# Kernel tuning notes

Hardware: AMD Instinct MI355X
Metric: run time of the kernel (lower is better)

## Reference

```python
import jax, jax.numpy as jnp
import numpy as np

B, N, F_ = 4, 2048, 512
H = 8
D = F_ // H


def setup_inputs() -> dict:
    key = jax.random.key(0)
    ks = jax.random.split(key, 9)
    s = 1.0 / np.sqrt(F_)
    return {
        "x": jax.random.normal(ks[0], (B, N, F_), dtype=jnp.float32),
        "Wq": jax.random.normal(ks[1], (F_, F_), dtype=jnp.float32) * s,
        "bq": jax.random.normal(ks[2], (F_,), dtype=jnp.float32) * 0.01,
        "Wk": jax.random.normal(ks[3], (F_, F_), dtype=jnp.float32) * s,
        "bk": jax.random.normal(ks[4], (F_,), dtype=jnp.float32) * 0.01,
        "Wv": jax.random.normal(ks[5], (F_, F_), dtype=jnp.float32) * s,
        "bv": jax.random.normal(ks[6], (F_,), dtype=jnp.float32) * 0.01,
        "Wo": jax.random.normal(ks[7], (F_, F_), dtype=jnp.float32) * s,
        "bo": jax.random.normal(ks[8], (F_,), dtype=jnp.float32) * 0.01,
    }


def reference(x, Wq, bq, Wk, bk, Wv, bv, Wo, bo):
    b, n, f = x.shape
    h, d = H, f // H
    # projections -> [b, h, n, d]
    q = (x @ Wq + bq).reshape(b, n, h, d).transpose(0, 2, 1, 3)
    k = (x @ Wk + bk).reshape(b, n, h, d).transpose(0, 2, 1, 3)
    v = (x @ Wv + bv).reshape(b, n, h, d).transpose(0, 2, 1, 3)
    # NOTE: module scales by sqrt(feats), not sqrt(head_dim)
    sqrt_d = jnp.asarray(f, x.dtype) ** 0.5
    score = jax.nn.softmax(jnp.einsum('bhif,bhjf->bhij', q, k) / sqrt_d, axis=-1)
    attn = jnp.einsum('bhij,bhjf->bihf', score, v).reshape(b, n, f)
    return attn @ Wo + bo
```

## Files before the change

kernel.cpp:

```cpp
#include <hip/hip_runtime.h>


typedef _Float16 f16;
typedef _Float16 f16x2 __attribute__((ext_vector_type(2)));
typedef _Float16 f16x4 __attribute__((ext_vector_type(4)));
typedef _Float16 f16x8 __attribute__((ext_vector_type(8)));
typedef float f32x4 __attribute__((ext_vector_type(4)));

#define MFMA16(a, b, c) __builtin_amdgcn_mfma_f32_16x16x32_f16((a), (b), (c), 0, 0, 0)
#if __has_builtin(__builtin_amdgcn_exp2f)
#define EXP2(x) __builtin_amdgcn_exp2f(x)
#else
#define EXP2(x) exp2f(x)
#endif
#define GLLDS16(gp, lp)                                                    \
  __builtin_amdgcn_global_load_lds(                                        \
      (const __attribute__((address_space(1))) unsigned int*)(gp),         \
      (__attribute__((address_space(3))) unsigned int*)(lp), 16, 0, 0)

#define QSCALE 0.0637587f

__global__ __launch_bounds__(256) void k_cvt_x(const float* __restrict__ x,
                                               f16* __restrict__ xb, int n4) {
  int i = blockIdx.x * 256 + threadIdx.x;
  const int stride = gridDim.x * 256;
  const float4* xp = (const float4*)x;
  f16x4* op = (f16x4*)xb;
  for (; i < n4; i += stride) {
    float4 v = xp[i];
    f16x4 o = {(f16)v.x, (f16)v.y, (f16)v.z, (f16)v.w};
    op[i] = o;
  }
}

__global__ __launch_bounds__(256) void k_cvt_w(const float* __restrict__ Wq,
                                               const float* __restrict__ Wk,
                                               const float* __restrict__ Wv,
                                               const float* __restrict__ Wo,
                                               f16* __restrict__ wt) {
  const int w = blockIdx.y;
  const float* W = (w == 0) ? Wq : (w == 1) ? Wk : (w == 2) ? Wv : Wo;
  const int j0 = (blockIdx.x >> 4) * 32;
  const int k0 = (blockIdx.x & 15) * 32;
  __shared__ float tl[32][33];
  const int tx = threadIdx.x & 31, ty = threadIdx.x >> 5;
#pragma unroll
  for (int i = 0; i < 32; i += 8)
    tl[ty + i][tx] = W[(size_t)(k0 + ty + i) * 512 + j0 + tx];
  __syncthreads();
#pragma unroll
  for (int i = 0; i < 32; i += 8)
    wt[(size_t)w * 262144 + (size_t)(j0 + ty + i) * 512 + (k0 + tx)] =
        (f16)tl[tx][ty + i];
}

template <int BN, int MODE>
__global__ __launch_bounds__(256) void k_gemm(
    const f16* __restrict__ A, const f16* __restrict__ Wb3,
    const float* __restrict__ bias0, const float* __restrict__ bias1,
    const float* __restrict__ bias2, f16* __restrict__ oQ, f16* __restrict__ oK,
    f16* __restrict__ oV, float* __restrict__ oOut) {
  __shared__ __align__(16) f16 a_lds[128 * 64];
  __shared__ __align__(16) f16 b_lds[BN * 64];
  const int t = threadIdx.x;
  const int lane = t & 63, wid = t >> 6;
  const int l15 = lane & 15, l4 = lane >> 4;
  constexpr int MT = (BN == 128) ? 4 : 2;
  const int mbase = (BN == 128) ? (wid >> 1) * 64 : wid * 32;
  const int nbase = (BN == 128) ? (wid & 1) * 64 : 0;
  const int m0 = blockIdx.x * 128;
  const int by = blockIdx.y;
  const int wsel = (MODE == 0) ? (by >> 2) : 0;
  const int n0l = (MODE == 0) ? ((by & 3) * 128) : (by * (BN == 64 ? 64 : 128));
  const f16* Wt = Wb3 + (size_t)wsel * 262144;

  const int srow = t >> 3;
  const int sswz = ((t & 7) ^ (srow & 7)) * 8;
  const f16* Ag = A + (size_t)(m0 + srow) * 512 + sswz;
  const f16* Bg = Wt + (size_t)(n0l + srow) * 512 + sswz;

  f32x4 acc[MT][4];
  const f32x4 z4 = {0.f, 0.f, 0.f, 0.f};
#pragma unroll
  for (int i = 0; i < MT; i++)
#pragma unroll
    for (int j = 0; j < 4; j++) acc[i][j] = z4;

  for (int k0 = 0; k0 < 512; k0 += 64) {
#pragma unroll
    for (int i = 0; i < 4; i++)
      GLLDS16(Ag + (size_t)i * 16384 + k0, &a_lds[i * 2048 + wid * 512]);
#pragma unroll
    for (int i = 0; i < BN / 32; i++)
      GLLDS16(Bg + (size_t)i * 16384 + k0, &b_lds[i * 2048 + wid * 512]);
    __syncthreads();
#pragma unroll
    for (int ks = 0; ks < 2; ks++) {
      const int rs = ((ks * 4 + l4) ^ (l15 & 7)) * 8;
      f16x8 af[MT], bf[4];
#pragma unroll
      for (int mt = 0; mt < MT; mt++)
        af[mt] = *(const f16x8*)&a_lds[(mbase + mt * 16 + l15) * 64 + rs];
#pragma unroll
      for (int nt = 0; nt < 4; nt++)
        bf[nt] = *(const f16x8*)&b_lds[(nbase + nt * 16 + l15) * 64 + rs];
      __builtin_amdgcn_s_setprio(1);
#pragma unroll
      for (int mt = 0; mt < MT; mt++)
#pragma unroll
        for (int nt = 0; nt < 4; nt++)
          acc[mt][nt] = MFMA16(af[mt], bf[nt], acc[mt][nt]);
      __builtin_amdgcn_s_setprio(0);
    }
    __syncthreads();
  }

  if (MODE == 1) {
#pragma unroll
    for (int mt = 0; mt < MT; mt++)
#pragma unroll
      for (int nt = 0; nt < 4; nt++) {
        const int row = m0 + mbase + mt * 16 + l4 * 4;
        const int col = n0l + nbase + nt * 16 + l15;
        const float bv = bias0[col];
#pragma unroll
        for (int r = 0; r < 4; r++)
          oOut[(size_t)(row + r) * 512 + col] = acc[mt][nt][r] + bv;
      }
  } else {
#pragma unroll
    for (int mt = 0; mt < MT; mt++)
#pragma unroll
      for (int nt = 0; nt < 4; nt++) {
        const int colg = by * 128 + nbase + nt * 16 + l15;
        const int w = colg >> 9, jj = colg & 511;
        const int h = jj >> 6, d = jj & 63;
        const float* bp = (w == 0) ? bias0 : (w == 1) ? bias1 : bias2;
        const float bv = bp[jj];
        const float scl = (w == 0) ? QSCALE : 1.0f;
        const int rowg = m0 + mbase + mt * 16 + l4 * 4;
        const int b = rowg >> 11, nn = rowg & 2047;
        if (w == 2) {
          const size_t vb = ((size_t)(b * 8 + h) * 64 + d) * 2048 + nn;
#pragma unroll
          for (int r = 0; r < 4; r++)
            oV[vb + r] = (f16)(acc[mt][nt][r] + bv);
        } else {
          f16* op = (w == 0) ? oQ : oK;
          const size_t base = ((size_t)(b * 8 + h) * 2048 + nn) * 64 + d;
#pragma unroll
          for (int r = 0; r < 4; r++)
            op[base + (size_t)r * 64] = (f16)((acc[mt][nt][r] + bv) * scl);
        }
      }
  }
}

__global__ __launch_bounds__(128, 4) void k_attn(const f16* __restrict__ Q,
                                                 const f16* __restrict__ K,
                                                 const f16* __restrict__ Vt,
                                                 f16* __restrict__ CTX) {
  __shared__ __align__(16) f16 k_lds[2][4096];
  __shared__ __align__(16) f16 v_lds[2][4096];
  const int t = threadIdx.x, wid = t >> 6, lane = t & 63;
  const int l15 = lane & 15, l4 = lane >> 4;
  const int bid = blockIdx.x;
  const int bh = (bid & 7) * 4 + (bid >> 8);
  const int qb = (bid >> 3) & 31;
  const int q0 = qb * 64 + wid * 32;
  const size_t kvb = (size_t)bh * (2048 * 64);

  f16x8 qf[2][2];
#pragma unroll
  for (int g = 0; g < 2; g++)
#pragma unroll
    for (int ks = 0; ks < 2; ks++)
      qf[g][ks] = *(const f16x8*)&Q[kvb + (size_t)(q0 + g * 16 + l15) * 64 +
                                    ks * 32 + l4 * 8];

  f32x4 oa[2][4];
  f32x4 lacc[2];
  const f32x4 z4 = {0.f, 0.f, 0.f, 0.f};
#pragma unroll
  for (int g = 0; g < 2; g++) {
    lacc[g] = z4;
#pragma unroll
    for (int dt = 0; dt < 4; dt++) oa[g][dt] = z4;
  }
  const f16 one = (f16)1.0f;
  const f16x8 ones = {one, one, one, one, one, one, one, one};

  const int kswz = ((lane & 7) ^ (lane >> 3)) * 8;
  const f16* Kgp[4];
  const f16* Vgp[4];
#pragma unroll
  for (int i = 0; i < 4; i++) {
    const int L = i * 16 + wid * 8 + (lane >> 3);
    const int pr = (L & 0x20) | ((L & 0x0C) << 1) | ((L & 0x10) >> 2) | (L & 3);
    Kgp[i] = K + kvb + (size_t)pr * 64 + kswz;
    Vgp[i] = Vt + kvb + (size_t)L * 2048 + kswz;
  }

#pragma unroll
  for (int i = 0; i < 4; i++) {
    GLLDS16(Kgp[i], &k_lds[0][i * 1024 + wid * 512]);
    GLLDS16(Vgp[i], &v_lds[0][i * 1024 + wid * 512]);
  }
  __syncthreads();

  int cur = 0;
  for (int it = 0; it < 32; ++it) {
    if (it < 31) {
      const size_t kb = (size_t)(it + 1) * 4096;
      const size_t vb = (size_t)(it + 1) * 64;
#pragma unroll
      for (int i = 0; i < 4; i++) {
        GLLDS16(Kgp[i] + kb, &k_lds[cur ^ 1][i * 1024 + wid * 512]);
        GLLDS16(Vgp[i] + vb, &v_lds[cur ^ 1][i * 1024 + wid * 512]);
      }
    }

    f32x4 st[2][4];
#pragma unroll
    for (int g = 0; g < 2; g++)
#pragma unroll
      for (int w = 0; w < 4; w++) st[g][w] = z4;
    const f16* kl = k_lds[cur];
#pragma unroll
    for (int ks = 0; ks < 2; ks++) {
      const int rs = ((ks * 4 + l4) ^ (l15 & 7)) * 8;
      f16x8 kf[4];
#pragma unroll
      for (int w = 0; w < 4; w++)
        kf[w] = *(const f16x8*)&kl[(w * 16 + l15) * 64 + rs];
      __builtin_amdgcn_s_setprio(1);
#pragma unroll
      for (int w = 0; w < 4; w++) {
        st[0][w] = MFMA16(kf[w], qf[0][ks], st[0][w]);
        st[1][w] = MFMA16(kf[w], qf[1][ks], st[1][w]);
      }
      __builtin_amdgcn_s_setprio(0);
    }

    f16x8 pa[2][2];
#pragma unroll
    for (int g = 0; g < 2; g++)
#pragma unroll
      for (int ks = 0; ks < 2; ks++) {
        f16x2 a0 = __builtin_bit_cast(
            f16x2, __builtin_amdgcn_cvt_pkrtz(EXP2(st[g][2 * ks][0]),
                                              EXP2(st[g][2 * ks][1])));
        f16x2 a1 = __builtin_bit_cast(
            f16x2, __builtin_amdgcn_cvt_pkrtz(EXP2(st[g][2 * ks][2]),
                                              EXP2(st[g][2 * ks][3])));
        f16x2 a2 = __builtin_bit_cast(
            f16x2, __builtin_amdgcn_cvt_pkrtz(EXP2(st[g][2 * ks + 1][0]),
                                              EXP2(st[g][2 * ks + 1][1])));
        f16x2 a3 = __builtin_bit_cast(
            f16x2, __builtin_amdgcn_cvt_pkrtz(EXP2(st[g][2 * ks + 1][2]),
                                              EXP2(st[g][2 * ks + 1][3])));
        f16x8 p;
        p[0] = a0[0]; p[1] = a0[1]; p[2] = a1[0]; p[3] = a1[1];
        p[4] = a2[0]; p[5] = a2[1]; p[6] = a3[0]; p[7] = a3[1];
        pa[g][ks] = p;
      }

    const f16* vl = v_lds[cur];
#pragma unroll
    for (int ks = 0; ks < 2; ks++) {
      __builtin_amdgcn_s_setprio(1);
      lacc[0] = MFMA16(pa[0][ks], ones, lacc[0]);
      lacc[1] = MFMA16(pa[1][ks], ones, lacc[1]);
#pragma unroll
      for (int dt = 0; dt < 4; dt++) {
        const f16x8 vf = *(const f16x8*)&vl[(dt * 16 + l15) * 64 +
                                            ((ks * 4 + l4) ^ (l15 & 7)) * 8];
        oa[0][dt] = MFMA16(pa[0][ks], vf, oa[0][dt]);
        oa[1][dt] = MFMA16(pa[1][ks], vf, oa[1][dt]);
      }
      __builtin_amdgcn_s_setprio(0);
    }
    __syncthreads();
    cur ^= 1;
  }

  const int b = bh >> 3, h = bh & 7;
#pragma unroll
  for (int g = 0; g < 2; g++)
#pragma unroll
    for (int r = 0; r < 4; r++) {
      const float inv = 1.0f / lacc[g][r];
      const int qrow = q0 + g * 16 + l4 * 4 + r;
#pragma unroll
      for (int dt = 0; dt < 4; dt++)
        CTX[(size_t)(b * 2048 + qrow) * 512 + h * 64 + dt * 16 + l15] =
            (f16)(oa[g][dt][r] * inv);
    }
}

extern "C" void kernel_launch(void* const* d_in, const int* in_sizes, int n_in,
                              void* d_out, int out_size, void* d_ws,
                              size_t ws_size, hipStream_t stream) {
  const float* x = (const float*)d_in[0];
  const float* Wq = (const float*)d_in[1];
  const float* bq = (const float*)d_in[2];
  const float* Wk = (const float*)d_in[3];
  const float* bk = (const float*)d_in[4];
  const float* Wv = (const float*)d_in[5];
  const float* bv = (const float*)d_in[6];
  const float* Wo = (const float*)d_in[7];
  const float* bo = (const float*)d_in[8];
  float* out = (float*)d_out;
  char* ws = (char*)d_ws;

  f16* xb = (f16*)(ws);
  f16* wt = (f16*)(ws + (size_t)(8u << 20));
  f16* Qb = (f16*)(ws + (size_t)(10u << 20));
  f16* Kb = (f16*)(ws + (size_t)(18u << 20));
  f16* Vt = (f16*)(ws + (size_t)(26u << 20));
  f16* CX = (f16*)(ws + (size_t)(34u << 20));

  k_cvt_x<<<dim3(2048), dim3(256), 0, stream>>>(x, xb, 1048576);
  k_cvt_w<<<dim3(256, 4), dim3(256), 0, stream>>>(Wq, Wk, Wv, Wo, wt);
  k_gemm<128, 0><<<dim3(64, 12), dim3(256), 0, stream>>>(
      xb, wt, bq, bk, bv, Qb, Kb, Vt, nullptr);
  k_attn<<<dim3(1024), dim3(128), 0, stream>>>(Qb, Kb, Vt, CX);
  k_gemm<64, 1><<<dim3(64, 8), dim3(256), 0, stream>>>(
      CX, wt + (size_t)3 * 262144, bo, nullptr, nullptr, nullptr, nullptr,
      nullptr, out);
}
```

Measured before the change: 96.95 us.

## Use 4-wave attention blocks with triple-buffered K/V and vmcnt-based waits

The attention kernel now runs 256-thread blocks that each cover 128 query rows, so every K/V tile loaded into LDS serves twice as many queries and the grid halves. K/V staging moves from double to triple buffering with a two-tile prefetch distance. The end-of-iteration __syncthreads is replaced by a partial s_waitcnt vmcnt plus a raw barrier, so the next tile's loads can stay in flight. The cost is more LDS per block (48KB) and fewer resident blocks, and correctness depends on the hand-counted vmcnt value.

```diff
diff --git a/kernel.cpp b/kernel.cpp
--- a/kernel.cpp
+++ b/kernel.cpp
@@ -156,18 +156,18 @@
   }
 }
 
-__global__ __launch_bounds__(128, 4) void k_attn(const f16* __restrict__ Q,
+__global__ __launch_bounds__(256, 2) void k_attn(const f16* __restrict__ Q,
                                                  const f16* __restrict__ K,
                                                  const f16* __restrict__ Vt,
                                                  f16* __restrict__ CTX) {
-  __shared__ __align__(16) f16 k_lds[2][4096];
-  __shared__ __align__(16) f16 v_lds[2][4096];
+  __shared__ __align__(16) f16 k_lds[3][4096];
+  __shared__ __align__(16) f16 v_lds[3][4096];
   const int t = threadIdx.x, wid = t >> 6, lane = t & 63;
   const int l15 = lane & 15, l4 = lane >> 4;
   const int bid = blockIdx.x;
-  const int bh = (bid & 7) * 4 + (bid >> 8);
-  const int qb = (bid >> 3) & 31;
-  const int q0 = qb * 64 + wid * 32;
+  const int bh = (bid & 7) * 4 + (bid >> 7);
+  const int qb = (bid >> 3) & 15;
+  const int q0 = qb * 128 + wid * 32;
   const size_t kvb = (size_t)bh * (2048 * 64);
 
   f16x8 qf[2][2];
@@ -190,34 +190,30 @@
   const f16 one = (f16)1.0f;
   const f16x8 ones = {one, one, one, one, one, one, one, one};
 
+  const int krow = wid * 8 + (lane >> 3);
   const int kswz = ((lane & 7) ^ (lane >> 3)) * 8;
-  const f16* Kgp[4];
-  const f16* Vgp[4];
-#pragma unroll
-  for (int i = 0; i < 4; i++) {
-    const int L = i * 16 + wid * 8 + (lane >> 3);
-    const int pr = (L & 0x20) | ((L & 0x0C) << 1) | ((L & 0x10) >> 2) | (L & 3);
-    Kgp[i] = K + kvb + (size_t)pr * 64 + kswz;
-    Vgp[i] = Vt + kvb + (size_t)L * 2048 + kswz;
-  }
-
-#pragma unroll
-  for (int i = 0; i < 4; i++) {
-    GLLDS16(Kgp[i], &k_lds[0][i * 1024 + wid * 512]);
-    GLLDS16(Vgp[i], &v_lds[0][i * 1024 + wid * 512]);
+  const int kperm = ((krow & 0x0C) << 1) | ((krow & 0x10) >> 2) | (krow & 3);
+  const f16* Kg = K + kvb + (size_t)kperm * 64 + kswz;
+  const f16* Vg = Vt + kvb + (size_t)krow * 2048 + kswz;
+
+#pragma unroll
+  for (int p = 0; p < 2; p++) {
+    GLLDS16(Kg + p * 4096, &k_lds[p][wid * 512]);
+    GLLDS16(Kg + p * 4096 + 2048, &k_lds[p][wid * 512 + 2048]);
+    GLLDS16(Vg + p * 64, &v_lds[p][wid * 512]);
+    GLLDS16(Vg + p * 64 + 32 * 2048, &v_lds[p][wid * 512 + 2048]);
   }
   __syncthreads();
 
-  int cur = 0;
+  int cur = 0, stg = 2;
   for (int it = 0; it < 32; ++it) {
-    if (it < 31) {
-      const size_t kb = (size_t)(it + 1) * 4096;
-      const size_t vb = (size_t)(it + 1) * 64;
-#pragma unroll
-      for (int i = 0; i < 4; i++) {
-        GLLDS16(Kgp[i] + kb, &k_lds[cur ^ 1][i * 1024 + wid * 512]);
-        GLLDS16(Vgp[i] + vb, &v_lds[cur ^ 1][i * 1024 + wid * 512]);
-      }
+    if (it < 30) {
+      const size_t kb = (size_t)(it + 2) * 4096;
+      const size_t vb = (size_t)(it + 2) * 64;
+      GLLDS16(Kg + kb, &k_lds[stg][wid * 512]);
+      GLLDS16(Kg + kb + 2048, &k_lds[stg][wid * 512 + 2048]);
+      GLLDS16(Vg + vb, &v_lds[stg][wid * 512]);
+      GLLDS16(Vg + vb + 32 * 2048, &v_lds[stg][wid * 512 + 2048]);
     }
 
     f32x4 st[2][4];
@@ -225,7 +221,7 @@
     for (int g = 0; g < 2; g++)
 #pragma unroll
       for (int w = 0; w < 4; w++) st[g][w] = z4;
-    const f16* kl = k_lds[cur];
+    const f16* kl = &k_lds[cur][0];
 #pragma unroll
     for (int ks = 0; ks < 2; ks++) {
       const int rs = ((ks * 4 + l4) ^ (l15 & 7)) * 8;
@@ -265,7 +261,7 @@
         pa[g][ks] = p;
       }
 
-    const f16* vl = v_lds[cur];
+    const f16* vl = &v_lds[cur][0];
 #pragma unroll
     for (int ks = 0; ks < 2; ks++) {
       __builtin_amdgcn_s_setprio(1);
@@ -280,8 +276,17 @@
       }
       __builtin_amdgcn_s_setprio(0);
     }
-    __syncthreads();
-    cur ^= 1;
+
+    if (it < 31) {
+      if (it < 30)
+        asm volatile("s_waitcnt vmcnt(4)" ::: "memory");
+      else
+        asm volatile("s_waitcnt vmcnt(0)" ::: "memory");
+      __builtin_amdgcn_s_barrier();
+      __builtin_amdgcn_sched_barrier(0);
+    }
+    cur = (cur == 2) ? 0 : cur + 1;
+    stg = (stg == 2) ? 0 : stg + 1;
   }
 
   const int b = bh >> 3, h = bh & 7;
@@ -324,7 +329,7 @@
   k_cvt_w<<<dim3(256, 4), dim3(256), 0, stream>>>(Wq, Wk, Wv, Wo, wt);
   k_gemm<128, 0><<<dim3(64, 12), dim3(256), 0, stream>>>(
       xb, wt, bq, bk, bv, Qb, Kb, Vt, nullptr);
-  k_attn<<<dim3(1024), dim3(128), 0, stream>>>(Qb, Kb, Vt, CX);
+  k_attn<<<dim3(512), dim3(256), 0, stream>>>(Qb, Kb, Vt, CX);
   k_gemm<64, 1><<<dim3(64, 8), dim3(256), 0, stream>>>(
       CX, wt + (size_t)3 * 262144, bo, nullptr, nullptr, nullptr, nullptr,
       nullptr, out);
```

Measured after the change: 84.66 us. 1.15x faster.

## Split attention KV range into two halves and add a combine kernel

Applied to the files above, without the earlier changes.

Each attention block now uses 4 waves covering 128 query rows and processes only half of the key/value sequence. Unnormalized partial outputs and row sums go to scratch, with the partials stored in the output buffer. A new combine kernel adds the two halves and normalizes before the output projection. The split gives twice as many waves per query tile and halves loop length per block, at the cost of an extra launch, partial-result memory traffic and f16 rounding of unnormalized partials.

```diff
diff --git a/kernel.cpp b/kernel.cpp
--- a/kernel.cpp
+++ b/kernel.cpp
@@ -156,19 +156,22 @@
   }
 }
 
-__global__ __launch_bounds__(128, 4) void k_attn(const f16* __restrict__ Q,
+__global__ __launch_bounds__(256, 4) void k_attn(const f16* __restrict__ Q,
                                                  const f16* __restrict__ K,
                                                  const f16* __restrict__ Vt,
-                                                 f16* __restrict__ CTX) {
+                                                 f16* __restrict__ Op,
+                                                 float* __restrict__ lp) {
   __shared__ __align__(16) f16 k_lds[2][4096];
   __shared__ __align__(16) f16 v_lds[2][4096];
   const int t = threadIdx.x, wid = t >> 6, lane = t & 63;
   const int l15 = lane & 15, l4 = lane >> 4;
   const int bid = blockIdx.x;
-  const int bh = (bid & 7) * 4 + (bid >> 8);
-  const int qb = (bid >> 3) & 31;
-  const int q0 = qb * 64 + wid * 32;
+  const int bh = (bid & 7) * 4 + ((bid >> 7) & 3);
+  const int qb = (bid >> 3) & 15;
+  const int s = bid >> 9;
+  const int q0 = qb * 128 + wid * 32;
   const size_t kvb = (size_t)bh * (2048 * 64);
+  const int kv0 = s * 1024;
 
   f16x8 qf[2][2];
 #pragma unroll
@@ -190,34 +193,27 @@
   const f16 one = (f16)1.0f;
   const f16x8 ones = {one, one, one, one, one, one, one, one};
 
+  const int krow = wid * 8 + (lane >> 3);
   const int kswz = ((lane & 7) ^ (lane >> 3)) * 8;
-  const f16* Kgp[4];
-  const f16* Vgp[4];
-#pragma unroll
-  for (int i = 0; i < 4; i++) {
-    const int L = i * 16 + wid * 8 + (lane >> 3);
-    const int pr = (L & 0x20) | ((L & 0x0C) << 1) | ((L & 0x10) >> 2) | (L & 3);
-    Kgp[i] = K + kvb + (size_t)pr * 64 + kswz;
-    Vgp[i] = Vt + kvb + (size_t)L * 2048 + kswz;
-  }
-
-#pragma unroll
-  for (int i = 0; i < 4; i++) {
-    GLLDS16(Kgp[i], &k_lds[0][i * 1024 + wid * 512]);
-    GLLDS16(Vgp[i], &v_lds[0][i * 1024 + wid * 512]);
-  }
+  const int kperm = ((krow & 0x0C) << 1) | ((krow & 0x10) >> 2) | (krow & 3);
+  const f16* Kg = K + kvb + (size_t)(kv0 + kperm) * 64 + kswz;
+  const f16* Vg = Vt + kvb + (size_t)krow * 2048 + kv0 + kswz;
+
+  GLLDS16(Kg, &k_lds[0][wid * 512]);
+  GLLDS16(Kg + 2048, &k_lds[0][wid * 512 + 2048]);
+  GLLDS16(Vg, &v_lds[0][wid * 512]);
+  GLLDS16(Vg + 32 * 2048, &v_lds[0][wid * 512 + 2048]);
   __syncthreads();
 
   int cur = 0;
-  for (int it = 0; it < 32; ++it) {
-    if (it < 31) {
+  for (int it = 0; it < 16; ++it) {
+    if (it < 15) {
       const size_t kb = (size_t)(it + 1) * 4096;
       const size_t vb = (size_t)(it + 1) * 64;
-#pragma unroll
-      for (int i = 0; i < 4; i++) {
-        GLLDS16(Kgp[i] + kb, &k_lds[cur ^ 1][i * 1024 + wid * 512]);
-        GLLDS16(Vgp[i] + vb, &v_lds[cur ^ 1][i * 1024 + wid * 512]);
-      }
+      GLLDS16(Kg + kb, &k_lds[cur ^ 1][wid * 512]);
+      GLLDS16(Kg + kb + 2048, &k_lds[cur ^ 1][wid * 512 + 2048]);
+      GLLDS16(Vg + vb, &v_lds[cur ^ 1][wid * 512]);
+      GLLDS16(Vg + vb + 32 * 2048, &v_lds[cur ^ 1][wid * 512 + 2048]);
     }
 
     f32x4 st[2][4];
@@ -225,7 +221,7 @@
     for (int g = 0; g < 2; g++)
 #pragma unroll
       for (int w = 0; w < 4; w++) st[g][w] = z4;
-    const f16* kl = k_lds[cur];
+    const f16* kl = &k_lds[cur][0];
 #pragma unroll
     for (int ks = 0; ks < 2; ks++) {
       const int rs = ((ks * 4 + l4) ^ (l15 & 7)) * 8;
@@ -265,7 +261,7 @@
         pa[g][ks] = p;
       }
 
-    const f16* vl = v_lds[cur];
+    const f16* vl = &v_lds[cur][0];
 #pragma unroll
     for (int ks = 0; ks < 2; ks++) {
       __builtin_amdgcn_s_setprio(1);
@@ -284,18 +280,34 @@
     cur ^= 1;
   }
 
+  const size_t sb = (size_t)(s * 32 + bh) * 2048;
+#pragma unroll
+  for (int g = 0; g < 2; g++)
+#pragma unroll
+    for (int r = 0; r < 4; r++) {
+      const int qrow = q0 + g * 16 + l4 * 4 + r;
+#pragma unroll
+      for (int dt = 0; dt < 4; dt++)
+        Op[(sb + qrow) * 64 + dt * 16 + l15] = (f16)oa[g][dt][r];
+      if (l15 == 0) lp[sb + qrow] = lacc[g][r];
+    }
+}
+
+__global__ __launch_bounds__(256) void k_comb(const f16* __restrict__ Op,
+                                              const float* __restrict__ lp,
+                                              f16* __restrict__ CX) {
+  const int tid = blockIdx.x * 256 + threadIdx.x;
+  const int row = tid >> 3;
+  const int d0 = (tid & 7) * 8;
+  const int bh = row >> 11, n = row & 2047;
+  const float inv = 1.0f / (lp[row] + lp[row + 65536]);
+  const f16x8 o0 = *(const f16x8*)&Op[(size_t)row * 64 + d0];
+  const f16x8 o1 = *(const f16x8*)&Op[(size_t)(row + 65536) * 64 + d0];
+  f16x8 o;
+#pragma unroll
+  for (int j = 0; j < 8; j++) o[j] = (f16)(((float)o0[j] + (float)o1[j]) * inv);
   const int b = bh >> 3, h = bh & 7;
-#pragma unroll
-  for (int g = 0; g < 2; g++)
-#pragma unroll
-    for (int r = 0; r < 4; r++) {
-      const float inv = 1.0f / lacc[g][r];
-      const int qrow = q0 + g * 16 + l4 * 4 + r;
-#pragma unroll
-      for (int dt = 0; dt < 4; dt++)
-        CTX[(size_t)(b * 2048 + qrow) * 512 + h * 64 + dt * 16 + l15] =
-            (f16)(oa[g][dt][r] * inv);
-    }
+  *(f16x8*)&CX[((size_t)(b * 2048 + n) * 512) + h * 64 + d0] = o;
 }
 
 extern "C" void kernel_launch(void* const* d_in, const int* in_sizes, int n_in,
@@ -319,12 +331,15 @@
   f16* Kb = (f16*)(ws + (size_t)(18u << 20));
   f16* Vt = (f16*)(ws + (size_t)(26u << 20));
   f16* CX = (f16*)(ws + (size_t)(34u << 20));
+  float* lps = (float*)(ws + (size_t)(42u << 20));
+  f16* Opart = (f16*)d_out;
 
   k_cvt_x<<<dim3(2048), dim3(256), 0, stream>>>(x, xb, 1048576);
   k_cvt_w<<<dim3(256, 4), dim3(256), 0, stream>>>(Wq, Wk, Wv, Wo, wt);
   k_gemm<128, 0><<<dim3(64, 12), dim3(256), 0, stream>>>(
       xb, wt, bq, bk, bv, Qb, Kb, Vt, nullptr);
-  k_attn<<<dim3(1024), dim3(128), 0, stream>>>(Qb, Kb, Vt, CX);
+  k_attn<<<dim3(1024), dim3(256), 0, stream>>>(Qb, Kb, Vt, Opart, lps);
+  k_comb<<<dim3(2048), dim3(256), 0, stream>>>(Opart, lps, CX);
   k_gemm<64, 1><<<dim3(64, 8), dim3(256), 0, stream>>>(
       CX, wt + (size_t)3 * 262144, bo, nullptr, nullptr, nullptr, nullptr,
       nullptr, out);
```

Result: faster. 90.61 us (-6.5%).

## Restructure attention to one wave per block with 32-key tiles and no barriers

Applied to the files above, without the earlier changes.

The attention kernel now runs one 64-lane wave per block. That wave owns all 64 query rows, so each K/V fragment read from LDS feeds four query groups instead of two. The KV tile shrinks to 32 keys with a double-buffered LDS ring, and the V swizzle is adjusted to match. Block-wide __syncthreads is replaced by explicit s_waitcnt vmcnt waits plus a sched_barrier, and the setprio hints are dropped. This aims to cut barrier stalls and LDS traffic per MFMA, at the cost of twice as many loop iterations, more accumulator registers, and less latency hiding per block.

```diff
diff --git a/kernel.cpp b/kernel.cpp
--- a/kernel.cpp
+++ b/kernel.cpp
@@ -156,33 +156,33 @@
   }
 }
 
-__global__ __launch_bounds__(128, 4) void k_attn(const f16* __restrict__ Q,
-                                                 const f16* __restrict__ K,
-                                                 const f16* __restrict__ Vt,
-                                                 f16* __restrict__ CTX) {
-  __shared__ __align__(16) f16 k_lds[2][4096];
-  __shared__ __align__(16) f16 v_lds[2][4096];
-  const int t = threadIdx.x, wid = t >> 6, lane = t & 63;
+__global__ __launch_bounds__(64) void k_attn(const f16* __restrict__ Q,
+                                             const f16* __restrict__ K,
+                                             const f16* __restrict__ Vt,
+                                             f16* __restrict__ CTX) {
+  __shared__ __align__(16) f16 k_lds[2][2048];
+  __shared__ __align__(16) f16 v_lds[2][2048];
+  const int lane = threadIdx.x & 63;
   const int l15 = lane & 15, l4 = lane >> 4;
   const int bid = blockIdx.x;
   const int bh = (bid & 7) * 4 + (bid >> 8);
   const int qb = (bid >> 3) & 31;
-  const int q0 = qb * 64 + wid * 32;
+  const int q0 = qb * 64;
   const size_t kvb = (size_t)bh * (2048 * 64);
 
-  f16x8 qf[2][2];
-#pragma unroll
-  for (int g = 0; g < 2; g++)
+  f16x8 qf[4][2];
+#pragma unroll
+  for (int g = 0; g < 4; g++)
 #pragma unroll
     for (int ks = 0; ks < 2; ks++)
       qf[g][ks] = *(const f16x8*)&Q[kvb + (size_t)(q0 + g * 16 + l15) * 64 +
                                     ks * 32 + l4 * 8];
 
-  f32x4 oa[2][4];
-  f32x4 lacc[2];
+  f32x4 oa[4][4];
+  f32x4 lacc[4];
   const f32x4 z4 = {0.f, 0.f, 0.f, 0.f};
 #pragma unroll
-  for (int g = 0; g < 2; g++) {
+  for (int g = 0; g < 4; g++) {
     lacc[g] = z4;
 #pragma unroll
     for (int dt = 0; dt < 4; dt++) oa[g][dt] = z4;
@@ -190,103 +190,98 @@
   const f16 one = (f16)1.0f;
   const f16x8 ones = {one, one, one, one, one, one, one, one};
 
-  const int kswz = ((lane & 7) ^ (lane >> 3)) * 8;
-  const f16* Kgp[4];
-  const f16* Vgp[4];
+  int koff[4], voff[4];
 #pragma unroll
   for (int i = 0; i < 4; i++) {
-    const int L = i * 16 + wid * 8 + (lane >> 3);
-    const int pr = (L & 0x20) | ((L & 0x0C) << 1) | ((L & 0x10) >> 2) | (L & 3);
-    Kgp[i] = K + kvb + (size_t)pr * 64 + kswz;
-    Vgp[i] = Vt + kvb + (size_t)L * 2048 + kswz;
-  }
+    const int L = i * 8 + (lane >> 3);
+    const int piL = ((L >> 2) & 3) * 8 + ((L >> 4) & 1) * 4 + (L & 3);
+    const int kslot = (lane & 7) ^ (L & 7);
+    koff[i] = piL * 64 + kslot * 8;
+    const int d = i * 16 + (lane >> 2);
+    const int vslot = (lane & 3) ^ (d & 3);
+    voff[i] = d * 2048 + vslot * 8;
+  }
+  const f16* Kbh = K + kvb;
+  const f16* Vbh = Vt + kvb;
 
 #pragma unroll
   for (int i = 0; i < 4; i++) {
-    GLLDS16(Kgp[i], &k_lds[0][i * 1024 + wid * 512]);
-    GLLDS16(Vgp[i], &v_lds[0][i * 1024 + wid * 512]);
-  }
-  __syncthreads();
-
-  int cur = 0;
-  for (int it = 0; it < 32; ++it) {
-    if (it < 31) {
-      const size_t kb = (size_t)(it + 1) * 4096;
-      const size_t vb = (size_t)(it + 1) * 64;
+    GLLDS16(Kbh + koff[i], &k_lds[0][i * 512]);
+    GLLDS16(Vbh + voff[i], &v_lds[0][i * 512]);
+  }
+
+  for (int it = 0; it < 64; ++it) {
+    const int cur = it & 1;
+    if (it < 63) {
+      const int kadv = (it + 1) * 2048;
+      const int vadv = (it + 1) * 32;
 #pragma unroll
       for (int i = 0; i < 4; i++) {
-        GLLDS16(Kgp[i] + kb, &k_lds[cur ^ 1][i * 1024 + wid * 512]);
-        GLLDS16(Vgp[i] + vb, &v_lds[cur ^ 1][i * 1024 + wid * 512]);
+        GLLDS16(Kbh + koff[i] + kadv, &k_lds[cur ^ 1][i * 512]);
+        GLLDS16(Vbh + voff[i] + vadv, &v_lds[cur ^ 1][i * 512]);
       }
-    }
-
-    f32x4 st[2][4];
-#pragma unroll
-    for (int g = 0; g < 2; g++)
-#pragma unroll
-      for (int w = 0; w < 4; w++) st[g][w] = z4;
-    const f16* kl = k_lds[cur];
+      asm volatile("s_waitcnt vmcnt(8)" ::: "memory");
+    } else {
+      asm volatile("s_waitcnt vmcnt(0)" ::: "memory");
+    }
+    __builtin_amdgcn_sched_barrier(0);
+
+    f32x4 st[4][2];
+#pragma unroll
+    for (int g = 0; g < 4; g++)
+#pragma unroll
+      for (int w = 0; w < 2; w++) st[g][w] = z4;
+    const f16* kl = &k_lds[cur][0];
 #pragma unroll
     for (int ks = 0; ks < 2; ks++) {
       const int rs = ((ks * 4 + l4) ^ (l15 & 7)) * 8;
-      f16x8 kf[4];
-#pragma unroll
-      for (int w = 0; w < 4; w++)
+      f16x8 kf[2];
+#pragma unroll
+      for (int w = 0; w < 2; w++)
         kf[w] = *(const f16x8*)&kl[(w * 16 + l15) * 64 + rs];
-      __builtin_amdgcn_s_setprio(1);
-#pragma unroll
-      for (int w = 0; w < 4; w++) {
-        st[0][w] = MFMA16(kf[w], qf[0][ks], st[0][w]);
-        st[1][w] = MFMA16(kf[w], qf[1][ks], st[1][w]);
-      }
-      __builtin_amdgcn_s_setprio(0);
-    }
-
-    f16x8 pa[2][2];
-#pragma unroll
-    for (int g = 0; g < 2; g++)
-#pragma unroll
-      for (int ks = 0; ks < 2; ks++) {
-        f16x2 a0 = __builtin_bit_cast(
-            f16x2, __builtin_amdgcn_cvt_pkrtz(EXP2(st[g][2 * ks][0]),
-                                              EXP2(st[g][2 * ks][1])));
-        f16x2 a1 = __builtin_bit_cast(
-            f16x2, __builtin_amdgcn_cvt_pkrtz(EXP2(st[g][2 * ks][2]),
-                                              EXP2(st[g][2 * ks][3])));
-        f16x2 a2 = __builtin_bit_cast(
-            f16x2, __builtin_amdgcn_cvt_pkrtz(EXP2(st[g][2 * ks + 1][0]),
-                                              EXP2(st[g][2 * ks + 1][1])));
-        f16x2 a3 = __builtin_bit_cast(
-            f16x2, __builtin_amdgcn_cvt_pkrtz(EXP2(st[g][2 * ks + 1][2]),
-                                              EXP2(st[g][2 * ks + 1][3])));
-        f16x8 p;
-        p[0] = a0[0]; p[1] = a0[1]; p[2] = a1[0]; p[3] = a1[1];
-        p[4] = a2[0]; p[5] = a2[1]; p[6] = a3[0]; p[7] = a3[1];
-        pa[g][ks] = p;
-      }
-
-    const f16* vl = v_lds[cur];
-#pragma unroll
-    for (int ks = 0; ks < 2; ks++) {
-      __builtin_amdgcn_s_setprio(1);
-      lacc[0] = MFMA16(pa[0][ks], ones, lacc[0]);
-      lacc[1] = MFMA16(pa[1][ks], ones, lacc[1]);
-#pragma unroll
-      for (int dt = 0; dt < 4; dt++) {
-        const f16x8 vf = *(const f16x8*)&vl[(dt * 16 + l15) * 64 +
-                                            ((ks * 4 + l4) ^ (l15 & 7)) * 8];
-        oa[0][dt] = MFMA16(pa[0][ks], vf, oa[0][dt]);
-        oa[1][dt] = MFMA16(pa[1][ks], vf, oa[1][dt]);
-      }
-      __builtin_amdgcn_s_setprio(0);
-    }
-    __syncthreads();
-    cur ^= 1;
+#pragma unroll
+      for (int w = 0; w < 2; w++)
+#pragma unroll
+        for (int g = 0; g < 4; g++)
+          st[g][w] = MFMA16(kf[w], qf[g][ks], st[g][w]);
+    }
+
+    f16x8 pa[4];
+#pragma unroll
+    for (int g = 0; g < 4; g++) {
+      f16x2 a0 = __builtin_bit_cast(
+          f16x2,
+          __builtin_amdgcn_cvt_pkrtz(EXP2(st[g][0][0]), EXP2(st[g][0][1])));
+      f16x2 a1 = __builtin_bit_cast(
+          f16x2,
+          __builtin_amdgcn_cvt_pkrtz(EXP2(st[g][0][2]), EXP2(st[g][0][3])));
+      f16x2 a2 = __builtin_bit_cast(
+          f16x2,
+          __builtin_amdgcn_cvt_pkrtz(EXP2(st[g][1][0]), EXP2(st[g][1][1])));
+      f16x2 a3 = __builtin_bit_cast(
+          f16x2,
+          __builtin_amdgcn_cvt_pkrtz(EXP2(st[g][1][2]), EXP2(st[g][1][3])));
+      f16x8 p;
+      p[0] = a0[0]; p[1] = a0[1]; p[2] = a1[0]; p[3] = a1[1];
+      p[4] = a2[0]; p[5] = a2[1]; p[6] = a3[0]; p[7] = a3[1];
+      pa[g] = p;
+    }
+
+    const f16* vl = &v_lds[cur][0];
+#pragma unroll
+    for (int g = 0; g < 4; g++) lacc[g] = MFMA16(pa[g], ones, lacc[g]);
+#pragma unroll
+    for (int dt = 0; dt < 4; dt++) {
+      const f16x8 vf = *(const f16x8*)&vl[(dt * 16 + l15) * 32 +
+                                          ((l4 ^ (l15 & 3)) * 8)];
+#pragma unroll
+      for (int g = 0; g < 4; g++) oa[g][dt] = MFMA16(pa[g], vf, oa[g][dt]);
+    }
   }
 
   const int b = bh >> 3, h = bh & 7;
 #pragma unroll
-  for (int g = 0; g < 2; g++)
+  for (int g = 0; g < 4; g++)
 #pragma unroll
     for (int r = 0; r < 4; r++) {
       const float inv = 1.0f / lacc[g][r];
@@ -324,7 +319,7 @@
   k_cvt_w<<<dim3(256, 4), dim3(256), 0, stream>>>(Wq, Wk, Wv, Wo, wt);
   k_gemm<128, 0><<<dim3(64, 12), dim3(256), 0, stream>>>(
       xb, wt, bq, bk, bv, Qb, Kb, Vt, nullptr);
-  k_attn<<<dim3(1024), dim3(128), 0, stream>>>(Qb, Kb, Vt, CX);
+  k_attn<<<dim3(1024), dim3(64), 0, stream>>>(Qb, Kb, Vt, CX);
   k_gemm<64, 1><<<dim3(64, 8), dim3(256), 0, stream>>>(
       CX, wt + (size_t)3 * 262144, bo, nullptr, nullptr, nullptr, nullptr,
       nullptr, out);
```

Result: slower. 114.3 us (+17.9%).
